# Optimization experiments

Measured on AMD Instinct MI355X. Metric: run time of the kernel, lower is better.

Reference implementation:

```python
import jax, jax.numpy as jnp
import numpy as np

B, S, D = 2, 2048, 2048
H, KVH, HD = 16, 4, 128
NREP = H // KVH  # GQA repeat factor


def _rope(x, cos, sin):
    # x: [B,S,h,HD]; pairs (x[2k], x[2k+1]) form complex numbers
    xr = x[..., 0::2]
    xi = x[..., 1::2]
    cos = cos[None, :, None, :]  # [1,S,1,HD/2]
    sin = sin[None, :, None, :]
    out_r = xr * cos - xi * sin
    out_i = xr * sin + xi * cos
    return jnp.stack([out_r, out_i], axis=-1).reshape(x.shape)


def setup_inputs() -> dict:
    key = jax.random.key(0)
    ks = jax.random.split(key, 5)
    x = jax.random.normal(ks[0], (B, S, D), dtype=jnp.float32)
    # standard rotary frequencies
    inv_freq = 1.0 / (10000.0 ** (np.arange(0, HD, 2, dtype=np.float64) / HD))
    ang = np.outer(np.arange(S, dtype=np.float64), inv_freq)
    freqs_cos = jnp.asarray(np.cos(ang), dtype=jnp.float32)  # [S, HD/2]
    freqs_sin = jnp.asarray(np.sin(ang), dtype=jnp.float32)
    wq = jax.random.normal(ks[1], (D, H * HD), dtype=jnp.float32) * 0.02
    wk = jax.random.normal(ks[2], (D, KVH * HD), dtype=jnp.float32) * 0.02
    wv = jax.random.normal(ks[3], (D, KVH * HD), dtype=jnp.float32) * 0.02
    wo = jax.random.normal(ks[4], (H * HD, D), dtype=jnp.float32) * 0.02
    cache_k = jnp.zeros((B, S, KVH, HD), dtype=jnp.float32)
    cache_v = jnp.zeros((B, S, KVH, HD), dtype=jnp.float32)
    return {"x": x, "freqs_cos": freqs_cos, "freqs_sin": freqs_sin,
            "wq": wq, "wk": wk, "wv": wv, "wo": wo,
            "cache_k": cache_k, "cache_v": cache_v, "start_pos": 0}


def reference(x, freqs_cos, freqs_sin, wq, wk, wv, wo, cache_k, cache_v, start_pos):
    b, s, _ = x.shape
    xq = (x @ wq).reshape(b, s, H, HD)
    xk = (x @ wk).reshape(b, s, KVH, HD)
    xv = (x @ wv).reshape(b, s, KVH, HD)
    xq = _rope(xq, freqs_cos, freqs_sin)
    xk = _rope(xk, freqs_cos, freqs_sin)
    # KV cache update + slice (start_pos is a static Python int)
    ck = cache_k.at[:, start_pos:start_pos + s].set(xk)
    cv = cache_v.at[:, start_pos:start_pos + s].set(xv)
    keys = ck[:, :start_pos + s]    # [B,T,KVH,HD]
    vals = cv[:, :start_pos + s]
    # GQA without materializing repeat_kv: group query heads per kv head
    q = xq.reshape(b, s, KVH, NREP, HD)
    scores = jnp.einsum('bsknd,btkd->bknst', q, keys) / np.float32(np.sqrt(HD))
    probs = jax.nn.softmax(scores.astype(jnp.float32), axis=-1).astype(x.dtype)
    out = jnp.einsum('bknst,btkd->bsknd', probs, vals).reshape(b, s, H * HD)
    return out @ wo
```

## Files before the change

kernel.cpp:

```cpp
#include <hip/hip_runtime.h>
#include <stdint.h>
#include <stddef.h>

#define S_LEN  2048
#define NH     16
#define NKVH   4
#define HD_    128
#define DMODEL 2048
#define NQKV   3072
#define MROWS  4096

typedef __attribute__((ext_vector_type(8)))  __bf16 bf16x8;
typedef __attribute__((ext_vector_type(4)))  __bf16 bf16x4;
typedef __attribute__((ext_vector_type(4)))  float  f32x4;
typedef __attribute__((ext_vector_type(16))) float  f32x16;

#define MFMA16(a, b, c) __builtin_amdgcn_mfma_f32_16x16x32_bf16((a), (b), (c), 0, 0, 0)
#define MFMA32(a, b, c) __builtin_amdgcn_mfma_f32_32x32x16_bf16((a), (b), (c), 0, 0, 0)

__device__ __forceinline__ void gload16(const void* g, void* l) {
  __builtin_amdgcn_global_load_lds((const __attribute__((address_space(1))) void*)g,
                                   (__attribute__((address_space(3))) void*)l,
                                   16, 0, 0);
}

__device__ __forceinline__ uint32_t cvtpk(float lo, float hi) {
  uint32_t d;
  asm("v_cvt_pk_bf16_f32 %0, %1, %2" : "=v"(d) : "v"(lo), "v"(hi));
  return d;
}
__device__ __forceinline__ void pswap(uint32_t& a, uint32_t& b) {
  asm("s_nop 1\n\tv_permlane32_swap_b32 %0, %1" : "+v"(a), "+v"(b));
}
__device__ __forceinline__ float fast_exp2(float x) {
  float r;
  asm("v_exp_f32 %0, %1\n\ts_nop 0" : "=v"(r) : "v"(x));
  return r;
}

__global__ void prep_kernel(const float* __restrict__ x, __bf16* __restrict__ xb,
                            const float* __restrict__ wq, const float* __restrict__ wk,
                            const float* __restrict__ wv, const float* __restrict__ wo,
                            __bf16* __restrict__ wqkvT, __bf16* __restrict__ woT) {
  __shared__ float tile[64][65];
  const int bid = blockIdx.x;
  const int tid = threadIdx.x;
  if (bid < 8192) {
    size_t i = (size_t)bid * 256 + tid;
    const float4* xv = (const float4*)x;
    float4 v = xv[i];
    bf16x4 o;
    o[0] = (__bf16)v.x; o[1] = (__bf16)v.y; o[2] = (__bf16)v.z; o[3] = (__bf16)v.w;
    *(bf16x4*)(xb + i * 4) = o;
    return;
  }
  int b2 = bid - 8192;
  const float* W; __bf16* WT; int ldw, kx, ny;
  if (b2 < 1024)      { W = wq; WT = wqkvT;                        ldw = 2048; kx = b2 & 31; ny = b2 >> 5; }
  else if (b2 < 1280) { int t = b2 - 1024; W = wk; WT = wqkvT + (size_t)2048 * 2048; ldw = 512; kx = t & 31; ny = t >> 5; }
  else if (b2 < 1536) { int t = b2 - 1280; W = wv; WT = wqkvT + (size_t)2560 * 2048; ldw = 512; kx = t & 31; ny = t >> 5; }
  else                { int t = b2 - 1536; W = wo; WT = woT;       ldw = 2048; kx = t & 31; ny = t >> 5; }
  const int k0 = kx * 64, n0 = ny * 64;
#pragma unroll
  for (int r = 0; r < 16; ++r) {
    int idx = r * 256 + tid;
    int kr = idx >> 6, nc = idx & 63;
    tile[kr][nc] = W[(size_t)(k0 + kr) * ldw + n0 + nc];
  }
  __syncthreads();
#pragma unroll
  for (int r = 0; r < 16; ++r) {
    int idx = r * 256 + tid;
    int nr = idx >> 6, kc = idx & 63;
    WT[(size_t)(n0 + nr) * 2048 + k0 + kc] = (__bf16)tile[kc][nr];
  }
}

template <int MODE>
__global__ __launch_bounds__(256, 2) void gemm_kernel(
    const __bf16* __restrict__ A, int lda,
    const __bf16* __restrict__ Bt, int ldb,
    void* __restrict__ Cout, int ldc, int Kdim,
    const float* __restrict__ fc, const float* __restrict__ fs,
    __bf16* __restrict__ xq, __bf16* __restrict__ Kp, __bf16* __restrict__ VTp) {
  __shared__ __attribute__((aligned(16))) __bf16 As[128 * 64];
  __shared__ __attribute__((aligned(16))) __bf16 Bs[128 * 64];
  const int tid = threadIdx.x;
  const int w = tid >> 6, l = tid & 63, lg = l >> 4, lr = l & 15;
  const int wm = w >> 1, wn = w & 1;
  const int m0 = blockIdx.y * 128, n0 = blockIdx.x * 128;

  f32x4 acc[4][4] = {};

  for (int k0 = 0; k0 < Kdim; k0 += 64) {
#pragma unroll
    for (int t = 0; t < 4; ++t) {
      int o = (t * 256 + tid) * 16;
      int row = o >> 7;
      int slot = (o >> 4) & 7;
      int sw = slot ^ (row & 7);
      gload16(A + (size_t)(m0 + row) * lda + k0 + sw * 8,
              (char*)As + t * 4096 + (w << 10));
      gload16(Bt + (size_t)(n0 + row) * ldb + k0 + sw * 8,
              (char*)Bs + t * 4096 + (w << 10));
    }
    __syncthreads();
#pragma unroll
    for (int c = 0; c < 2; ++c) {
      bf16x8 af[4];
#pragma unroll
      for (int mi = 0; mi < 4; ++mi) {
        int row = wm * 64 + mi * 16 + lr;
        int slot = (c * 4 + lg) ^ (row & 7);
        af[mi] = *(const bf16x8*)((const char*)As + row * 128 + slot * 16);
      }
#pragma unroll
      for (int ni = 0; ni < 4; ++ni) {
        int rn = wn * 64 + ni * 16 + lr;
        int slot = (c * 4 + lg) ^ (rn & 7);
        bf16x8 bfr = *(const bf16x8*)((const char*)Bs + rn * 128 + slot * 16);
#pragma unroll
        for (int mi = 0; mi < 4; ++mi)
          acc[mi][ni] = MFMA16(af[mi], bfr, acc[mi][ni]);
      }
    }
    __syncthreads();
  }

  if (MODE == 1) {
    const float qs = 0.12755102871936672f;
    if (n0 < 2560) {
#pragma unroll
      for (int mi = 0; mi < 4; ++mi)
#pragma unroll
        for (int ni = 0; ni < 4; ++ni)
#pragma unroll
          for (int i = 0; i < 4; ++i) {
            float v = acc[mi][ni][i];
            float p = __shfl_xor(v, 1);
            int cc = n0 + wn * 64 + ni * 16 + lr;
            int r  = m0 + wm * 64 + mi * 16 + lg * 4 + i;
            int s  = r & (S_LEN - 1);
            int j  = (cc & 127) >> 1;
            float c = fc[s * 64 + j], sn = fs[s * 64 + j];
            float o = (lr & 1) ? (p * sn + v * c)
                               : (v * c - p * sn);
            if (n0 < DMODEL) {
              xq[(size_t)r * DMODEL + cc] = (__bf16)(o * qs);
            } else {
              int bb = r >> 11, kt = s >> 6, rr = s & 63;
              int kvh = (cc - DMODEL) >> 7, dk = (cc - DMODEL) & 127;
              size_t e = ((size_t)((bb * 4 + kvh) * 32 + kt) * 16 + (dk >> 3)) * 512
                         + rr * 8 + (dk & 7);
              Kp[e] = (__bf16)o;
            }
          }
    } else {
#pragma unroll
      for (int mi = 0; mi < 4; ++mi)
#pragma unroll
        for (int ni = 0; ni < 4; ++ni)
#pragma unroll
          for (int i = 0; i < 4; ++i) {
            float v = acc[mi][ni][i];
            int cc = n0 + wn * 64 + ni * 16 + lr;
            int r  = m0 + wm * 64 + mi * 16 + lg * 4 + i;
            int s  = r & (S_LEN - 1);
            int bb = r >> 11, kt = s >> 6, rr = s & 63;
            int kvh = (cc - 2560) >> 7, d = (cc - 2560) & 127;
            size_t e = ((size_t)((bb * 4 + kvh) * 32 + kt) * 8 + (rr >> 3)) * 1024
                       + d * 8 + (rr & 7);
            VTp[e] = (__bf16)v;
          }
    }
    return;
  }

#pragma unroll
  for (int mi = 0; mi < 4; ++mi)
#pragma unroll
    for (int ni = 0; ni < 4; ++ni)
#pragma unroll
      for (int i = 0; i < 4; ++i) {
        int r = m0 + wm * 64 + mi * 16 + lg * 4 + i;
        int cc = n0 + wn * 64 + ni * 16 + lr;
        ((float*)Cout)[(size_t)r * ldc + cc] = acc[mi][ni][i];
      }
}

__global__ __launch_bounds__(256, 2) void attn_kernel(
    const __bf16* __restrict__ xq, const __bf16* __restrict__ Kp,
    const __bf16* __restrict__ VTp, __bf16* __restrict__ out) {
  __shared__ __attribute__((aligned(16))) __bf16 Ks0[64 * 128];
  __shared__ __attribute__((aligned(16))) __bf16 Ks1[64 * 128];
  __shared__ __attribute__((aligned(16))) __bf16 Vs0[128 * 64];
  __shared__ __attribute__((aligned(16))) __bf16 Vs1[128 * 64];
  const int tid = threadIdx.x;
  const int w = tid >> 6, l = tid & 63;
  const int qc = l & 31, hi = l >> 5;
  const int bh = blockIdx.y;
  const int b = bh >> 4, h = bh & 15, kvh = h >> 2;
  const int bkv = b * NKVH + kvh;
  const int q0 = blockIdx.x * 128 + w * 32;

  const __bf16* Ktiles = Kp  + (size_t)bkv * 32 * 8192;
  const __bf16* Vtiles = VTp + (size_t)bkv * 32 * 8192;

  auto stage = [&](int kt, __bf16* ksb, __bf16* vsb) {
    const __bf16* ksrc = Ktiles + (size_t)kt * 8192;
    const __bf16* vsrc = Vtiles + (size_t)kt * 8192;
#pragma unroll
    for (int t = 0; t < 4; ++t) {
      gload16(ksrc + (t * 256 + tid) * 8, (char*)ksb + t * 4096 + (w << 10));
      gload16(vsrc + (t * 256 + tid) * 8, (char*)vsb + t * 4096 + (w << 10));
    }
  };

  bf16x8 aq[8];
#pragma unroll
  for (int c = 0; c < 8; ++c)
    aq[c] = *(const bf16x8*)(xq + (size_t)(b * S_LEN + q0 + qc) * DMODEL +
                             h * HD_ + c * 16 + hi * 8);

  f32x16 o_acc[4] = {};
  float m = -1e30f, lsum = 0.0f;

  typedef union { uint32_t u[4]; bf16x8 v; } pfrag_t;

  auto tile_step = [&](const __bf16* ksb, const __bf16* vsb) {
    const char* kb = (const char*)ksb + hi * 1024 + qc * 16;
    const char* vb = (const char*)vsb + hi * 2048 + qc * 16;

    f32x16 st[2] = {};
    __builtin_amdgcn_s_setprio(1);
#pragma unroll
    for (int t = 0; t < 2; ++t) {
#pragma unroll
      for (int c = 0; c < 8; ++c) {
        bf16x8 kf = *(const bf16x8*)(kb + c * 2048 + t * 512);
        st[t] = MFMA32(kf, aq[c], st[t]);
      }
    }
    __builtin_amdgcn_s_setprio(0);

    float pm = st[0][0];
#pragma unroll
    for (int t = 0; t < 2; ++t)
#pragma unroll
      for (int r = 0; r < 16; ++r) pm = fmaxf(pm, st[t][r]);
    pm = fmaxf(pm, __shfl_xor(pm, 32));

    if (__any(pm - m > 11.54f)) {
      float mn = fmaxf(m, pm);
      float sf = fast_exp2(m - mn);
      lsum *= sf;
#pragma unroll
      for (int dt = 0; dt < 4; ++dt)
#pragma unroll
        for (int r = 0; r < 16; ++r) o_acc[dt][r] *= sf;
      m = mn;
    }

    float rsum = 0.0f;
#pragma unroll
    for (int t = 0; t < 2; ++t)
#pragma unroll
      for (int r = 0; r < 16; ++r) {
        st[t][r] = fast_exp2(st[t][r] - m);
        rsum += st[t][r];
      }
    rsum += __shfl_xor(rsum, 32);
    lsum += rsum;

    pfrag_t pf[4];
#pragma unroll
    for (int t = 0; t < 2; ++t)
#pragma unroll
      for (int half = 0; half < 2; ++half) {
        int bs = half * 8;
        uint32_t x0 = cvtpk(st[t][bs + 0], st[t][bs + 1]);
        uint32_t y0 = cvtpk(st[t][bs + 4], st[t][bs + 5]);
        uint32_t x1 = cvtpk(st[t][bs + 2], st[t][bs + 3]);
        uint32_t y1 = cvtpk(st[t][bs + 6], st[t][bs + 7]);
        pswap(x0, y0);
        pswap(x1, y1);
        pf[t * 2 + half].u[0] = x0;
        pf[t * 2 + half].u[1] = x1;
        pf[t * 2 + half].u[2] = y0;
        pf[t * 2 + half].u[3] = y1;
      }

    __builtin_amdgcn_s_setprio(1);
#pragma unroll
    for (int dt = 0; dt < 4; ++dt) {
#pragma unroll
      for (int ks = 0; ks < 4; ++ks) {
        bf16x8 vf = *(const bf16x8*)(vb + ks * 4096 + dt * 512);
        o_acc[dt] = MFMA32(vf, pf[ks].v, o_acc[dt]);
      }
    }
    __builtin_amdgcn_s_setprio(0);
  };

  stage(0, Ks0, Vs0);
  __syncthreads();

#pragma unroll 1
  for (int kt = 0; kt < S_LEN / 64; kt += 2) {
    stage(kt + 1, Ks1, Vs1);
    tile_step(Ks0, Vs0);
    __syncthreads();
    if (kt + 2 < S_LEN / 64) stage(kt + 2, Ks0, Vs0);
    tile_step(Ks1, Vs1);
    __syncthreads();
  }

  float rinv = 1.0f / lsum;
  const size_t orow = (size_t)(b * S_LEN + q0 + qc) * DMODEL + h * HD_;
#pragma unroll
  for (int dt = 0; dt < 4; ++dt)
#pragma unroll
    for (int rg = 0; rg < 4; ++rg) {
      bf16x4 ov;
#pragma unroll
      for (int i = 0; i < 4; ++i)
        ov[i] = (__bf16)(o_acc[dt][rg * 4 + i] * rinv);
      int d = dt * 32 + rg * 8 + hi * 4;
      *(bf16x4*)(out + orow + d) = ov;
    }
}

extern "C" void kernel_launch(void* const* d_in, const int* in_sizes, int n_in,
                              void* d_out, int out_size, void* d_ws, size_t ws_size,
                              hipStream_t stream) {
  const float* x  = (const float*)d_in[0];
  const float* fc = (const float*)d_in[1];
  const float* fs = (const float*)d_in[2];
  const float* wq = (const float*)d_in[3];
  const float* wk = (const float*)d_in[4];
  const float* wv = (const float*)d_in[5];
  const float* wo = (const float*)d_in[6];

  char* ws = (char*)d_ws;
  __bf16* xb    = (__bf16*)(ws);
  __bf16* wqkvT = (__bf16*)(ws + (16u << 20));
  __bf16* woT   = (__bf16*)(ws + (28u << 20));
  __bf16* xq    = (__bf16*)(ws + (36u << 20));
  __bf16* Kp    = (__bf16*)(ws + (52u << 20));
  __bf16* VTp   = (__bf16*)(ws + (56u << 20));

  prep_kernel<<<10752, 256, 0, stream>>>(x, xb, wq, wk, wv, wo, wqkvT, woT);
  {
    dim3 g(NQKV / 128, MROWS / 128);
    gemm_kernel<1><<<g, 256, 0, stream>>>(xb, 2048, wqkvT, 2048, nullptr, 0, 2048,
                                          fc, fs, xq, Kp, VTp);
  }
  {
    dim3 g(S_LEN / 128, 32);
    attn_kernel<<<g, 256, 0, stream>>>(xq, Kp, VTp, xb);
  }
  {
    dim3 g(DMODEL / 128, MROWS / 128);
    gemm_kernel<0><<<g, 256, 0, stream>>>(xb, 2048, woT, 2048, d_out, 2048, 2048,
                                          fc, fs, nullptr, nullptr, nullptr);
  }
}
```

Before: 194.4 us.

## Software-pipeline QK^T of next tile with softmax and PV of current tile

Splits the attention tile step into a QK^T phase and a softmax+PV phase. K and V are staged separately, and the next tile's QK^T MFMAs are issued before the current tile's softmax and PV so that matrix and vector work can interleave. The max and sum reductions become trees to shorten dependency chains. This keeps two score accumulators live, which raises register pressure under launch_bounds(256,2).

```diff
diff --git a/kernel.cpp b/kernel.cpp
--- a/kernel.cpp
+++ b/kernel.cpp
@@ -206,14 +206,17 @@
   const __bf16* Ktiles = Kp  + (size_t)bkv * 32 * 8192;
   const __bf16* Vtiles = VTp + (size_t)bkv * 32 * 8192;
 
-  auto stage = [&](int kt, __bf16* ksb, __bf16* vsb) {
+  auto stageK = [&](int kt, __bf16* ksb) {
     const __bf16* ksrc = Ktiles + (size_t)kt * 8192;
+#pragma unroll
+    for (int t = 0; t < 4; ++t)
+      gload16(ksrc + (t * 256 + tid) * 8, (char*)ksb + t * 4096 + (w << 10));
+  };
+  auto stageV = [&](int kt, __bf16* vsb) {
     const __bf16* vsrc = Vtiles + (size_t)kt * 8192;
 #pragma unroll
-    for (int t = 0; t < 4; ++t) {
-      gload16(ksrc + (t * 256 + tid) * 8, (char*)ksb + t * 4096 + (w << 10));
+    for (int t = 0; t < 4; ++t)
       gload16(vsrc + (t * 256 + tid) * 8, (char*)vsb + t * 4096 + (w << 10));
-    }
   };
 
   bf16x8 aq[8];
@@ -227,11 +230,10 @@
 
   typedef union { uint32_t u[4]; bf16x8 v; } pfrag_t;
 
-  auto tile_step = [&](const __bf16* ksb, const __bf16* vsb) {
+  auto qk = [&](const __bf16* ksb, f32x16 (&st)[2]) {
     const char* kb = (const char*)ksb + hi * 1024 + qc * 16;
-    const char* vb = (const char*)vsb + hi * 2048 + qc * 16;
-
-    f32x16 st[2] = {};
+    st[0] = (f32x16)0.0f;
+    st[1] = (f32x16)0.0f;
     __builtin_amdgcn_s_setprio(1);
 #pragma unroll
     for (int t = 0; t < 2; ++t) {
@@ -242,12 +244,20 @@
       }
     }
     __builtin_amdgcn_s_setprio(0);
-
-    float pm = st[0][0];
-#pragma unroll
-    for (int t = 0; t < 2; ++t)
-#pragma unroll
-      for (int r = 0; r < 16; ++r) pm = fmaxf(pm, st[t][r]);
+  };
+
+  auto finish_pv = [&](f32x16 (&st)[2], const __bf16* vsb) {
+    const char* vb = (const char*)vsb + hi * 2048 + qc * 16;
+
+    float mx0[8];
+#pragma unroll
+    for (int i = 0; i < 8; ++i)
+      mx0[i] = fmaxf(fmaxf(st[0][2 * i], st[0][2 * i + 1]),
+                     fmaxf(st[1][2 * i], st[1][2 * i + 1]));
+    float mx1[4];
+#pragma unroll
+    for (int i = 0; i < 4; ++i) mx1[i] = fmaxf(mx0[2 * i], mx0[2 * i + 1]);
+    float pm = fmaxf(fmaxf(mx1[0], mx1[1]), fmaxf(mx1[2], mx1[3]));
     pm = fmaxf(pm, __shfl_xor(pm, 32));
 
     if (__any(pm - m > 11.54f)) {
@@ -261,14 +271,22 @@
       m = mn;
     }
 
-    float rsum = 0.0f;
 #pragma unroll
     for (int t = 0; t < 2; ++t)
 #pragma unroll
-      for (int r = 0; r < 16; ++r) {
+      for (int r = 0; r < 16; ++r)
         st[t][r] = fast_exp2(st[t][r] - m);
-        rsum += st[t][r];
-      }
+
+    float s0[16];
+#pragma unroll
+    for (int i = 0; i < 16; ++i) s0[i] = st[0][i] + st[1][i];
+    float s1[8];
+#pragma unroll
+    for (int i = 0; i < 8; ++i) s1[i] = s0[2 * i] + s0[2 * i + 1];
+    float s2[4];
+#pragma unroll
+    for (int i = 0; i < 4; ++i) s2[i] = s1[2 * i] + s1[2 * i + 1];
+    float rsum = (s2[0] + s2[1]) + (s2[2] + s2[3]);
     rsum += __shfl_xor(rsum, 32);
     lsum += rsum;
 
@@ -302,16 +320,26 @@
     __builtin_amdgcn_s_setprio(0);
   };
 
-  stage(0, Ks0, Vs0);
+  f32x16 stA[2], stB[2];
+
+  stageK(0, Ks0);
+  stageV(0, Vs0);
   __syncthreads();
+  stageK(1, Ks1);
+  qk(Ks0, stA);
+  __syncthreads();
 
 #pragma unroll 1
-  for (int kt = 0; kt < S_LEN / 64; kt += 2) {
-    stage(kt + 1, Ks1, Vs1);
-    tile_step(Ks0, Vs0);
+  for (int t = 0; t < 32; t += 2) {
+    if (t + 2 < 32) stageK(t + 2, Ks0);
+    stageV(t + 1, Vs1);
+    qk(Ks1, stB);
+    finish_pv(stA, Vs0);
     __syncthreads();
-    if (kt + 2 < S_LEN / 64) stage(kt + 2, Ks0, Vs0);
-    tile_step(Ks1, Vs1);
+    if (t + 3 < 32) stageK(t + 3, Ks1);
+    if (t + 2 < 32) stageV(t + 2, Vs0);
+    if (t + 2 < 32) qk(Ks0, stA);
+    finish_pv(stB, Vs1);
     __syncthreads();
   }
 
```

Result: slower. 198.6 us (+2.2%).
